# Kernel optimization log

Hardware: AMD Instinct MI355X
Metric: run time of the kernel (lower is better)

## Reference

```python
import jax, jax.numpy as jnp
import numpy as np

# Material / problem parameters (from init_kwargs)
G_C = 0.0027
L_0 = 0.015
PF_TOL = 0.01
ENERGY_SCALING = 1.0
NU = 0.3
E_MOD = 210.0
LAM = E_MOD * NU / ((1.0 + NU) * (1.0 - 2.0 * NU))
MU = E_MOD / (2.0 * (1.0 + NU))
K_MOD = LAM + 2.0 * MU / 3.0  # bulk modulus for vol/dev split

N_NODES = 263169
N_ELEMS = 262144
N_IP = 4
NN = 4  # nodes per element


def setup_inputs() -> dict:
    key = jax.random.key(0)
    ks = jax.random.split(key, 9)
    u = jax.random.normal(ks[0], (N_NODES,), dtype=jnp.float32) * 0.01
    v = jax.random.normal(ks[1], (N_NODES,), dtype=jnp.float32) * 0.01
    c = jax.random.uniform(ks[2], (N_NODES,), dtype=jnp.float32)
    prev_c = jax.random.uniform(ks[3], (N_NODES,), dtype=jnp.float32)
    connectivities = jax.random.randint(ks[4], (N_ELEMS, NN), 0, N_NODES, dtype=jnp.int32)
    N = jax.random.uniform(ks[5], (N_ELEMS, N_IP, NN), dtype=jnp.float32)
    N = N / jnp.sum(N, axis=-1, keepdims=True)  # shape functions sum to 1
    dNdx = jax.random.normal(ks[6], (N_ELEMS, N_IP, 2, NN), dtype=jnp.float32)
    B = jax.random.normal(ks[7], (N_ELEMS, N_IP, 3, 2 * NN), dtype=jnp.float32)
    volumes = jax.random.uniform(ks[8], (N_ELEMS, N_IP), dtype=jnp.float32)
    return {"u": u, "v": v, "c": c, "prev_c": prev_c,
            "connectivities": connectivities, "N": N, "dNdx": dNdx,
            "B": B, "volumes": volumes}


def reference(u, v, c, prev_c, connectivities, N, dNdx, B, volumes):
    # --- phase-field gather + degradation -------------------------------
    c_el = c[connectivities]                     # [E, nn] irregular gather
    one_minus_c_el = 1.0 - c_el                  # c_elemental in source
    one_minus_c_ip = jnp.einsum('ein,en->ei', N, one_minus_c_el)  # [E, ip]
    ip_g = one_minus_c_ip ** 2                   # degradation g = (1-c)^2

    # --- fracture (AT2) energy density ----------------------------------
    c_ip = 1.0 - one_minus_c_ip
    grad_c = jnp.einsum('eidn,en->eid', dNdx, c_el)  # [E, ip, 2]
    frac_density = (G_C / (2.0 * L_0)) * (c_ip ** 2 + (L_0 ** 2) * jnp.sum(grad_c ** 2, axis=-1))
    E_fracture = jnp.sum(frac_density * volumes)

    # --- irreversibility penalty ----------------------------------------
    penalty = G_C / L_0 * (1.0 / PF_TOL ** 2 - 1.0) * ENERGY_SCALING
    E_irr = jnp.sum(0.5 * penalty * jax.nn.relu(prev_c - c) ** 2)

    # --- B-matrix strain transform --------------------------------------
    u_el = u[connectivities]                     # [E, nn]
    v_el = v[connectivities]                     # [E, nn]
    uv = jnp.stack((u_el, v_el), axis=-1).reshape(u_el.shape[0], 2 * NN)  # interleaved dofs
    strain = jnp.einsum('eikn,en->eik', B, uv)   # Voigt [E, ip, 3]
    exx, eyy, gxy = strain[..., 0], strain[..., 1], strain[..., 2]
    exy = 0.5 * gxy
    tr = exx + eyy                               # plane strain: ezz = 0

    # --- vol/dev (Amor) split energy parts ------------------------------
    dev_xx = exx - tr / 3.0
    dev_yy = eyy - tr / 3.0
    dev_zz = -tr / 3.0
    dev2 = dev_xx ** 2 + dev_yy ** 2 + dev_zz ** 2 + 2.0 * exy ** 2
    tr_pos = jnp.maximum(tr, 0.0)
    tr_neg = jnp.minimum(tr, 0.0)
    psi_plus = 0.5 * K_MOD * tr_pos ** 2 + MU * dev2
    psi_minus = 0.5 * K_MOD * tr_neg ** 2

    ip_strain_energy = (psi_plus * ip_g + psi_minus) * volumes
    E_elastic = jnp.sum(ip_strain_energy)
    return (E_elastic, E_fracture, E_irr)
```

## Files before the change

### kernel.cpp

```cpp
#include <hip/hip_runtime.h>

namespace {
constexpr int N_ELEMS  = 262144;
constexpr int N_NODES  = 263169;
constexpr int N_WORK   = N_ELEMS * 4;
constexpr int NTHREADS = N_WORK / 2;
constexpr int BLK      = 256;
constexpr int NBLOCKS  = NTHREADS / BLK;

constexpr float GC_2L0  = 0.09f;
constexpr float L0SQ    = 0.015f * 0.015f;
constexpr float MU_     = 80.76923076923077f;
constexpr float K_MOD   = 175.0f;
constexpr float PENALTY = 1799.82f;
}

typedef float vfloat4 __attribute__((ext_vector_type(4)));
typedef int   vint4   __attribute__((ext_vector_type(4)));

__device__ __forceinline__ float waveReduce(float x) {
#pragma unroll
    for (int off = 32; off; off >>= 1) x += __shfl_down(x, off, 64);
    return x;
}

__global__ __launch_bounds__(256) void fused_energy(
    const float* __restrict__ u, const float* __restrict__ v,
    const float* __restrict__ c, const float* __restrict__ prev_c,
    const int* __restrict__ conn,
    const float* __restrict__ Nf, const float* __restrict__ dNdx,
    const float* __restrict__ B, const float* __restrict__ vol,
    float* __restrict__ partials)
{
    const int tid = blockIdx.x * blockDim.x + threadIdx.x;
    const int u0 = tid, u1 = tid + NTHREADS;
    const int e0 = u0 >> 2, ip0 = u0 & 3;
    const int e1 = u1 >> 2, ip1 = u1 & 3;

    const vint4 cn0 = *reinterpret_cast<const vint4*>(conn + 4ll * e0);
    const vint4 cn1 = *reinterpret_cast<const vint4*>(conn + 4ll * e1);

    const vfloat4 Nr0 = *reinterpret_cast<const vfloat4*>(Nf + 16ll * e0 + 4 * ip0);
    const vfloat4 Nr1 = *reinterpret_cast<const vfloat4*>(Nf + 16ll * e1 + 4 * ip1);

    const float* Dp0 = dNdx + 32ll * e0 + 8 * ip0;
    const float* Dp1 = dNdx + 32ll * e1 + 8 * ip1;
    const vfloat4 dxa = *reinterpret_cast<const vfloat4*>(Dp0);
    const vfloat4 dya = *reinterpret_cast<const vfloat4*>(Dp0 + 4);
    const vfloat4 dxb = *reinterpret_cast<const vfloat4*>(Dp1);
    const vfloat4 dyb = *reinterpret_cast<const vfloat4*>(Dp1 + 4);

    const float* Bp0 = B + 96ll * e0 + 24 * ip0;
    const float* Bp1 = B + 96ll * e1 + 24 * ip1;
    const vfloat4 a0 = *reinterpret_cast<const vfloat4*>(Bp0 +  0);
    const vfloat4 a1 = *reinterpret_cast<const vfloat4*>(Bp0 +  4);
    const vfloat4 a2 = *reinterpret_cast<const vfloat4*>(Bp0 +  8);
    const vfloat4 a3 = *reinterpret_cast<const vfloat4*>(Bp0 + 12);
    const vfloat4 a4 = *reinterpret_cast<const vfloat4*>(Bp0 + 16);
    const vfloat4 a5 = *reinterpret_cast<const vfloat4*>(Bp0 + 20);
    const vfloat4 b0 = *reinterpret_cast<const vfloat4*>(Bp1 +  0);
    const vfloat4 b1 = *reinterpret_cast<const vfloat4*>(Bp1 +  4);
    const vfloat4 b2 = *reinterpret_cast<const vfloat4*>(Bp1 +  8);
    const vfloat4 b3 = *reinterpret_cast<const vfloat4*>(Bp1 + 12);
    const vfloat4 b4 = *reinterpret_cast<const vfloat4*>(Bp1 + 16);
    const vfloat4 b5 = *reinterpret_cast<const vfloat4*>(Bp1 + 20);
    const float vipa = vol[4ll * e0 + ip0];
    const float vipb = vol[4ll * e1 + ip1];

    float Eirr = 0.f;
    if (tid < N_NODES) {
        float d = fmaxf(prev_c[tid] - c[tid], 0.f);
        Eirr = 0.5f * PENALTY * d * d;
    }

    const float ca0 = c[cn0.x], ca1 = c[cn0.y], ca2 = c[cn0.z], ca3 = c[cn0.w];
    const float cb0 = c[cn1.x], cb1 = c[cn1.y], cb2 = c[cn1.z], cb3 = c[cn1.w];
    const float ua0 = u[cn0.x], va0 = v[cn0.x];
    const float ua1 = u[cn0.y], va1 = v[cn0.y];
    const float ua2 = u[cn0.z], va2 = v[cn0.z];
    const float ua3 = u[cn0.w], va3 = v[cn0.w];
    const float ub0 = u[cn1.x], vb0 = v[cn1.x];
    const float ub1 = u[cn1.y], vb1 = v[cn1.y];
    const float ub2 = u[cn1.z], vb2 = v[cn1.z];
    const float ub3 = u[cn1.w], vb3 = v[cn1.w];

    float Eel = 0.f, Efr = 0.f;
    {
        const float o0 = 1.f - ca0, o1 = 1.f - ca1, o2 = 1.f - ca2, o3 = 1.f - ca3;
        const float omc = Nr0.x * o0 + Nr0.y * o1 + Nr0.z * o2 + Nr0.w * o3;
        const float g = omc * omc, cip = 1.f - omc;
        const float gx = dxa.x * ca0 + dxa.y * ca1 + dxa.z * ca2 + dxa.w * ca3;
        const float gy = dya.x * ca0 + dya.y * ca1 + dya.z * ca2 + dya.w * ca3;
        Efr += GC_2L0 * (cip * cip + L0SQ * (gx * gx + gy * gy)) * vipa;
        const float exx = a0.x * ua0 + a0.y * va0 + a0.z * ua1 + a0.w * va1
                        + a1.x * ua2 + a1.y * va2 + a1.z * ua3 + a1.w * va3;
        const float eyy = a2.x * ua0 + a2.y * va0 + a2.z * ua1 + a2.w * va1
                        + a3.x * ua2 + a3.y * va2 + a3.z * ua3 + a3.w * va3;
        const float gxy = a4.x * ua0 + a4.y * va0 + a4.z * ua1 + a4.w * va1
                        + a5.x * ua2 + a5.y * va2 + a5.z * ua3 + a5.w * va3;
        const float exy = 0.5f * gxy;
        const float tr = exx + eyy, tr3 = tr * (1.f / 3.f);
        const float dxx = exx - tr3, dyy = eyy - tr3, dzz = -tr3;
        const float dev2 = dxx * dxx + dyy * dyy + dzz * dzz + 2.f * exy * exy;
        const float trp = fmaxf(tr, 0.f), trn = fminf(tr, 0.f);
        Eel += ((0.5f * K_MOD * trp * trp + MU_ * dev2) * g
                + 0.5f * K_MOD * trn * trn) * vipa;
    }
    {
        const float o0 = 1.f - cb0, o1 = 1.f - cb1, o2 = 1.f - cb2, o3 = 1.f - cb3;
        const float omc = Nr1.x * o0 + Nr1.y * o1 + Nr1.z * o2 + Nr1.w * o3;
        const float g = omc * omc, cip = 1.f - omc;
        const float gx = dxb.x * cb0 + dxb.y * cb1 + dxb.z * cb2 + dxb.w * cb3;
        const float gy = dyb.x * cb0 + dyb.y * cb1 + dyb.z * cb2 + dyb.w * cb3;
        Efr += GC_2L0 * (cip * cip + L0SQ * (gx * gx + gy * gy)) * vipb;
        const float exx = b0.x * ub0 + b0.y * vb0 + b0.z * ub1 + b0.w * vb1
                        + b1.x * ub2 + b1.y * vb2 + b1.z * ub3 + b1.w * vb3;
        const float eyy = b2.x * ub0 + b2.y * vb0 + b2.z * ub1 + b2.w * vb1
                        + b3.x * ub2 + b3.y * vb2 + b3.z * ub3 + b3.w * vb3;
        const float gxy = b4.x * ub0 + b4.y * vb0 + b4.z * ub1 + b4.w * vb1
                        + b5.x * ub2 + b5.y * vb2 + b5.z * ub3 + b5.w * vb3;
        const float exy = 0.5f * gxy;
        const float tr = exx + eyy, tr3 = tr * (1.f / 3.f);
        const float dxx = exx - tr3, dyy = eyy - tr3, dzz = -tr3;
        const float dev2 = dxx * dxx + dyy * dyy + dzz * dzz + 2.f * exy * exy;
        const float trp = fmaxf(tr, 0.f), trn = fminf(tr, 0.f);
        Eel += ((0.5f * K_MOD * trp * trp + MU_ * dev2) * g
                + 0.5f * K_MOD * trn * trn) * vipb;
    }

    Eel  = waveReduce(Eel);
    Efr  = waveReduce(Efr);
    Eirr = waveReduce(Eirr);
    __shared__ float sE[4], sF[4], sI[4];
    const int lane = threadIdx.x & 63, wid = threadIdx.x >> 6;
    if (lane == 0) { sE[wid] = Eel; sF[wid] = Efr; sI[wid] = Eirr; }
    __syncthreads();
    if (threadIdx.x == 0) {
        float* p = partials + 3ll * blockIdx.x;
        p[0] = sE[0] + sE[1] + sE[2] + sE[3];
        p[1] = sF[0] + sF[1] + sF[2] + sF[3];
        p[2] = sI[0] + sI[1] + sI[2] + sI[3];
    }
}

__global__ __launch_bounds__(256) void final_reduce(
    const float* __restrict__ partials, float* __restrict__ out)
{
    float s0 = 0.f, s1 = 0.f, s2 = 0.f;
    for (int i = threadIdx.x; i < NBLOCKS; i += 256) {
        const float* p = partials + 3ll * i;
        s0 += p[0]; s1 += p[1]; s2 += p[2];
    }
    s0 = waveReduce(s0);
    s1 = waveReduce(s1);
    s2 = waveReduce(s2);
    __shared__ float sA[4], sB[4], sC[4];
    const int lane = threadIdx.x & 63, wid = threadIdx.x >> 6;
    if (lane == 0) { sA[wid] = s0; sB[wid] = s1; sC[wid] = s2; }
    __syncthreads();
    if (threadIdx.x == 0) {
        out[0] = sA[0] + sA[1] + sA[2] + sA[3];
        out[1] = sB[0] + sB[1] + sB[2] + sB[3];
        out[2] = sC[0] + sC[1] + sC[2] + sC[3];
    }
}

extern "C" void kernel_launch(void* const* d_in, const int* in_sizes, int n_in,
                              void* d_out, int out_size, void* d_ws, size_t ws_size,
                              hipStream_t stream) {
    const float* u      = (const float*)d_in[0];
    const float* v      = (const float*)d_in[1];
    const float* c      = (const float*)d_in[2];
    const float* prev_c = (const float*)d_in[3];
    const int*   conn   = (const int*)d_in[4];
    const float* Nf     = (const float*)d_in[5];
    const float* dNdx   = (const float*)d_in[6];
    const float* B      = (const float*)d_in[7];
    const float* vol    = (const float*)d_in[8];
    float* out      = (float*)d_out;
    float* partials = (float*)d_ws;

    fused_energy<<<NBLOCKS, BLK, 0, stream>>>(
        u, v, c, prev_c, conn, Nf, dNdx, B, vol, partials);
    final_reduce<<<1, BLK, 0, stream>>>(partials, out);
}
```

Baseline: 50.91 us.

## Pair threads per element and share gathered node values via lane shuffles

The kernel changes its mapping so that two adjacent threads each handle two integration points of the same element, instead of each thread handling two unrelated points. The pair splits the irregular gathers: the even lane loads c and two u values, the odd lane loads v and the other two u values, and they exchange them with xor shuffles. This cuts the random gather count per element from 12 per point to 12 per element, removing redundant scattered memory traffic. In exchange it adds shuffles and selects, and the per-thread loads of N, dNdx and B become strided across the element.

```diff
diff --git a/kernel.cpp b/kernel.cpp
--- a/kernel.cpp
+++ b/kernel.cpp
@@ -3,8 +3,7 @@
 namespace {
 constexpr int N_ELEMS  = 262144;
 constexpr int N_NODES  = 263169;
-constexpr int N_WORK   = N_ELEMS * 4;
-constexpr int NTHREADS = N_WORK / 2;
+constexpr int NTHREADS = N_ELEMS * 2;
 constexpr int BLK      = 256;
 constexpr int NBLOCKS  = NTHREADS / BLK;
 
@@ -32,100 +31,109 @@
     const float* __restrict__ B, const float* __restrict__ vol,
     float* __restrict__ partials)
 {
-    const int tid = blockIdx.x * blockDim.x + threadIdx.x;
-    const int u0 = tid, u1 = tid + NTHREADS;
-    const int e0 = u0 >> 2, ip0 = u0 & 3;
-    const int e1 = u1 >> 2, ip1 = u1 & 3;
+    const int t = blockIdx.x * blockDim.x + threadIdx.x;
+    const int e    = t >> 1;
+    const int iplo = t & 1;
+    const bool ev  = (iplo == 0);
 
-    const vint4 cn0 = *reinterpret_cast<const vint4*>(conn + 4ll * e0);
-    const vint4 cn1 = *reinterpret_cast<const vint4*>(conn + 4ll * e1);
+    const vint4 cn = *reinterpret_cast<const vint4*>(conn + 4ll * e);
 
-    const vfloat4 Nr0 = *reinterpret_cast<const vfloat4*>(Nf + 16ll * e0 + 4 * ip0);
-    const vfloat4 Nr1 = *reinterpret_cast<const vfloat4*>(Nf + 16ll * e1 + 4 * ip1);
+    const vfloat4 NrA = *reinterpret_cast<const vfloat4*>(Nf + 16ll * e + 4 * iplo);
+    const vfloat4 NrB = *reinterpret_cast<const vfloat4*>(Nf + 16ll * e + 4 * iplo + 8);
 
-    const float* Dp0 = dNdx + 32ll * e0 + 8 * ip0;
-    const float* Dp1 = dNdx + 32ll * e1 + 8 * ip1;
-    const vfloat4 dxa = *reinterpret_cast<const vfloat4*>(Dp0);
-    const vfloat4 dya = *reinterpret_cast<const vfloat4*>(Dp0 + 4);
-    const vfloat4 dxb = *reinterpret_cast<const vfloat4*>(Dp1);
-    const vfloat4 dyb = *reinterpret_cast<const vfloat4*>(Dp1 + 4);
+    const float* Dp = dNdx + 32ll * e + 8 * iplo;
+    const vfloat4 dxA = *reinterpret_cast<const vfloat4*>(Dp);
+    const vfloat4 dyA = *reinterpret_cast<const vfloat4*>(Dp + 4);
+    const vfloat4 dxB = *reinterpret_cast<const vfloat4*>(Dp + 16);
+    const vfloat4 dyB = *reinterpret_cast<const vfloat4*>(Dp + 20);
 
-    const float* Bp0 = B + 96ll * e0 + 24 * ip0;
-    const float* Bp1 = B + 96ll * e1 + 24 * ip1;
-    const vfloat4 a0 = *reinterpret_cast<const vfloat4*>(Bp0 +  0);
-    const vfloat4 a1 = *reinterpret_cast<const vfloat4*>(Bp0 +  4);
-    const vfloat4 a2 = *reinterpret_cast<const vfloat4*>(Bp0 +  8);
-    const vfloat4 a3 = *reinterpret_cast<const vfloat4*>(Bp0 + 12);
-    const vfloat4 a4 = *reinterpret_cast<const vfloat4*>(Bp0 + 16);
-    const vfloat4 a5 = *reinterpret_cast<const vfloat4*>(Bp0 + 20);
-    const vfloat4 b0 = *reinterpret_cast<const vfloat4*>(Bp1 +  0);
-    const vfloat4 b1 = *reinterpret_cast<const vfloat4*>(Bp1 +  4);
-    const vfloat4 b2 = *reinterpret_cast<const vfloat4*>(Bp1 +  8);
-    const vfloat4 b3 = *reinterpret_cast<const vfloat4*>(Bp1 + 12);
-    const vfloat4 b4 = *reinterpret_cast<const vfloat4*>(Bp1 + 16);
-    const vfloat4 b5 = *reinterpret_cast<const vfloat4*>(Bp1 + 20);
-    const float vipa = vol[4ll * e0 + ip0];
-    const float vipb = vol[4ll * e1 + ip1];
+    const float* Bp = B + 96ll * e + 24 * iplo;
+    const vfloat4 a0 = *reinterpret_cast<const vfloat4*>(Bp +  0);
+    const vfloat4 a1 = *reinterpret_cast<const vfloat4*>(Bp +  4);
+    const vfloat4 a2 = *reinterpret_cast<const vfloat4*>(Bp +  8);
+    const vfloat4 a3 = *reinterpret_cast<const vfloat4*>(Bp + 12);
+    const vfloat4 a4 = *reinterpret_cast<const vfloat4*>(Bp + 16);
+    const vfloat4 a5 = *reinterpret_cast<const vfloat4*>(Bp + 20);
+    const vfloat4 q0 = *reinterpret_cast<const vfloat4*>(Bp + 48);
+    const vfloat4 q1 = *reinterpret_cast<const vfloat4*>(Bp + 52);
+    const vfloat4 q2 = *reinterpret_cast<const vfloat4*>(Bp + 56);
+    const vfloat4 q3 = *reinterpret_cast<const vfloat4*>(Bp + 60);
+    const vfloat4 q4 = *reinterpret_cast<const vfloat4*>(Bp + 64);
+    const vfloat4 q5 = *reinterpret_cast<const vfloat4*>(Bp + 68);
+
+    const float vipA = vol[4ll * e + iplo];
+    const float vipB = vol[4ll * e + iplo + 2];
 
     float Eirr = 0.f;
-    if (tid < N_NODES) {
-        float d = fmaxf(prev_c[tid] - c[tid], 0.f);
+    if (t < N_NODES) {
+        float d = fmaxf(prev_c[t] - c[t], 0.f);
         Eirr = 0.5f * PENALTY * d * d;
     }
 
-    const float ca0 = c[cn0.x], ca1 = c[cn0.y], ca2 = c[cn0.z], ca3 = c[cn0.w];
-    const float cb0 = c[cn1.x], cb1 = c[cn1.y], cb2 = c[cn1.z], cb3 = c[cn1.w];
-    const float ua0 = u[cn0.x], va0 = v[cn0.x];
-    const float ua1 = u[cn0.y], va1 = v[cn0.y];
-    const float ua2 = u[cn0.z], va2 = v[cn0.z];
-    const float ua3 = u[cn0.w], va3 = v[cn0.w];
-    const float ub0 = u[cn1.x], vb0 = v[cn1.x];
-    const float ub1 = u[cn1.y], vb1 = v[cn1.y];
-    const float ub2 = u[cn1.z], vb2 = v[cn1.z];
-    const float ub3 = u[cn1.w], vb3 = v[cn1.w];
+    const float* A  = ev ? c : v;
+    const int  idx4 = ev ? cn.x : cn.z;
+    const int  idx5 = ev ? cn.y : cn.w;
+    const float g0 = A[cn.x], g1 = A[cn.y], g2 = A[cn.z], g3 = A[cn.w];
+    const float g4 = u[idx4], g5 = u[idx5];
+
+    const float p0 = __shfl_xor(g0, 1);
+    const float p1 = __shfl_xor(g1, 1);
+    const float p2 = __shfl_xor(g2, 1);
+    const float p3 = __shfl_xor(g3, 1);
+    const float p4 = __shfl_xor(g4, 1);
+    const float p5 = __shfl_xor(g5, 1);
+
+    const float c0 = ev ? g0 : p0, c1 = ev ? g1 : p1;
+    const float c2 = ev ? g2 : p2, c3 = ev ? g3 : p3;
+    const float v0 = ev ? p0 : g0, v1 = ev ? p1 : g1;
+    const float v2 = ev ? p2 : g2, v3 = ev ? p3 : g3;
+    const float u0 = ev ? g4 : p4, u1 = ev ? g5 : p5;
+    const float u2 = ev ? p4 : g4, u3 = ev ? p5 : g5;
+
+    const float o0 = 1.f - c0, o1 = 1.f - c1, o2 = 1.f - c2, o3 = 1.f - c3;
 
     float Eel = 0.f, Efr = 0.f;
     {
-        const float o0 = 1.f - ca0, o1 = 1.f - ca1, o2 = 1.f - ca2, o3 = 1.f - ca3;
-        const float omc = Nr0.x * o0 + Nr0.y * o1 + Nr0.z * o2 + Nr0.w * o3;
+        const float omc = NrA.x * o0 + NrA.y * o1 + NrA.z * o2 + NrA.w * o3;
         const float g = omc * omc, cip = 1.f - omc;
-        const float gx = dxa.x * ca0 + dxa.y * ca1 + dxa.z * ca2 + dxa.w * ca3;
-        const float gy = dya.x * ca0 + dya.y * ca1 + dya.z * ca2 + dya.w * ca3;
-        Efr += GC_2L0 * (cip * cip + L0SQ * (gx * gx + gy * gy)) * vipa;
-        const float exx = a0.x * ua0 + a0.y * va0 + a0.z * ua1 + a0.w * va1
-                        + a1.x * ua2 + a1.y * va2 + a1.z * ua3 + a1.w * va3;
-        const float eyy = a2.x * ua0 + a2.y * va0 + a2.z * ua1 + a2.w * va1
-                        + a3.x * ua2 + a3.y * va2 + a3.z * ua3 + a3.w * va3;
-        const float gxy = a4.x * ua0 + a4.y * va0 + a4.z * ua1 + a4.w * va1
-                        + a5.x * ua2 + a5.y * va2 + a5.z * ua3 + a5.w * va3;
+        const float gx = dxA.x * c0 + dxA.y * c1 + dxA.z * c2 + dxA.w * c3;
+        const float gy = dyA.x * c0 + dyA.y * c1 + dyA.z * c2 + dyA.w * c3;
+        Efr += GC_2L0 * (cip * cip + L0SQ * (gx * gx + gy * gy)) * vipA;
+
+        const float exx = a0.x * u0 + a0.y * v0 + a0.z * u1 + a0.w * v1
+                        + a1.x * u2 + a1.y * v2 + a1.z * u3 + a1.w * v3;
+        const float eyy = a2.x * u0 + a2.y * v0 + a2.z * u1 + a2.w * v1
+                        + a3.x * u2 + a3.y * v2 + a3.z * u3 + a3.w * v3;
+        const float gxy = a4.x * u0 + a4.y * v0 + a4.z * u1 + a4.w * v1
+                        + a5.x * u2 + a5.y * v2 + a5.z * u3 + a5.w * v3;
         const float exy = 0.5f * gxy;
         const float tr = exx + eyy, tr3 = tr * (1.f / 3.f);
         const float dxx = exx - tr3, dyy = eyy - tr3, dzz = -tr3;
         const float dev2 = dxx * dxx + dyy * dyy + dzz * dzz + 2.f * exy * exy;
         const float trp = fmaxf(tr, 0.f), trn = fminf(tr, 0.f);
         Eel += ((0.5f * K_MOD * trp * trp + MU_ * dev2) * g
-                + 0.5f * K_MOD * trn * trn) * vipa;
+                + 0.5f * K_MOD * trn * trn) * vipA;
     }
     {
-        const float o0 = 1.f - cb0, o1 = 1.f - cb1, o2 = 1.f - cb2, o3 = 1.f - cb3;
-        const float omc = Nr1.x * o0 + Nr1.y * o1 + Nr1.z * o2 + Nr1.w * o3;
+        const float omc = NrB.x * o0 + NrB.y * o1 + NrB.z * o2 + NrB.w * o3;
         const float g = omc * omc, cip = 1.f - omc;
-        const float gx = dxb.x * cb0 + dxb.y * cb1 + dxb.z * cb2 + dxb.w * cb3;
-        const float gy = dyb.x * cb0 + dyb.y * cb1 + dyb.z * cb2 + dyb.w * cb3;
-        Efr += GC_2L0 * (cip * cip + L0SQ * (gx * gx + gy * gy)) * vipb;
-        const float exx = b0.x * ub0 + b0.y * vb0 + b0.z * ub1 + b0.w * vb1
-                        + b1.x * ub2 + b1.y * vb2 + b1.z * ub3 + b1.w * vb3;
-        const float eyy = b2.x * ub0 + b2.y * vb0 + b2.z * ub1 + b2.w * vb1
-                        + b3.x * ub2 + b3.y * vb2 + b3.z * ub3 + b3.w * vb3;
-        const float gxy = b4.x * ub0 + b4.y * vb0 + b4.z * ub1 + b4.w * vb1
-                        + b5.x * ub2 + b5.y * vb2 + b5.z * ub3 + b5.w * vb3;
+        const float gx = dxB.x * c0 + dxB.y * c1 + dxB.z * c2 + dxB.w * c3;
+        const float gy = dyB.x * c0 + dyB.y * c1 + dyB.z * c2 + dyB.w * c3;
+        Efr += GC_2L0 * (cip * cip + L0SQ * (gx * gx + gy * gy)) * vipB;
+
+        const float exx = q0.x * u0 + q0.y * v0 + q0.z * u1 + q0.w * v1
+                        + q1.x * u2 + q1.y * v2 + q1.z * u3 + q1.w * v3;
+        const float eyy = q2.x * u0 + q2.y * v0 + q2.z * u1 + q2.w * v1
+                        + q3.x * u2 + q3.y * v2 + q3.z * u3 + q3.w * v3;
+        const float gxy = q4.x * u0 + q4.y * v0 + q4.z * u1 + q4.w * v1
+                        + q5.x * u2 + q5.y * v2 + q5.z * u3 + q5.w * v3;
         const float exy = 0.5f * gxy;
         const float tr = exx + eyy, tr3 = tr * (1.f / 3.f);
         const float dxx = exx - tr3, dyy = eyy - tr3, dzz = -tr3;
         const float dev2 = dxx * dxx + dyy * dyy + dzz * dzz + 2.f * exy * exy;
         const float trp = fmaxf(tr, 0.f), trn = fminf(tr, 0.f);
         Eel += ((0.5f * K_MOD * trp * trp + MU_ * dev2) * g
-                + 0.5f * K_MOD * trn * trn) * vipb;
+                + 0.5f * K_MOD * trn * trn) * vipB;
     }
 
     Eel  = waveReduce(Eel);
```

Measured after the change: 48.12 us. -5.5%, faster.
